# Optimization experiments

Hardware: AMD Instinct MI355X
Metric: run time of the kernel (lower is better)

## Reference

```python
import jax, jax.numpy as jnp
import numpy as np
from jax import lax


def _conv1d(x, w, b):
    # x: [B,C,W], w: [Cout,Cin,K], b: [Cout]; SAME padding for K=3
    k = w.shape[-1]
    pad = (k - 1) // 2
    y = lax.conv_general_dilated(
        x, w, window_strides=(1,), padding=[(pad, pad)],
        dimension_numbers=("NCH", "OIH", "NCH"))
    return y + b[None, :, None]


def setup_inputs() -> dict:
    key = jax.random.key(0)
    k1, k2 = jax.random.split(key)
    B, C, H, W = 8, 64, 256, 256
    K = 3
    X = jax.random.normal(k1, (B, C, H, W), dtype=jnp.float32)
    W_conv = jax.random.normal(k2, (C, C, K), dtype=jnp.float32) * (1.0 / np.sqrt(C * K))
    b_conv = jnp.zeros((C,), dtype=jnp.float32)
    return {"X": X, "W_conv": W_conv, "b_conv": b_conv}


def reference(X, W_conv, b_conv):
    # SpatialConv, direction='down', inplace=True:
    #   Y[0] = X[0];  Y[i+1] = X[i+1] + tanh(conv1d(Y[i]))
    # (inplace updates mean each step reads the already-updated previous row)
    rows = jnp.transpose(X, (2, 0, 1, 3))  # [H,B,C,W]

    def step(prev_row, x_next):
        new_row = x_next + jnp.tanh(_conv1d(prev_row, W_conv, b_conv))
        return new_row, new_row

    y0 = rows[0]
    _, ys = lax.scan(step, y0, rows[1:])  # ys: [H-1,B,C,W]
    Y = jnp.concatenate([y0[None], ys], axis=0)  # [H,B,C,W]
    return jnp.transpose(Y, (1, 2, 0, 3))  # [B,C,H,W]
```

## Files before the change

kernel.cpp:

```cpp
#include <hip/hip_runtime.h>

typedef __bf16 bf16x8 __attribute__((ext_vector_type(8)));
typedef __bf16 bf16x4 __attribute__((ext_vector_type(4)));
typedef float  f32x4  __attribute__((ext_vector_type(4)));

#define NB 8
#define NC 64
#define NH 256
#define NW 256
#define NT 16
#define WT 16
#define SEG 32
#define NS 5
#define LDSW 82
#define LDSC 72

__device__ __forceinline__ float fast_tanh(float x) {
    float e = __expf(2.0f * x);
    return 1.0f - 2.0f / (1.0f + e);
}

__global__ __launch_bounds__(256, 1)
void spconv_trap(const float* __restrict__ Xg,
                 const float* __restrict__ Wg,
                 const float* __restrict__ Bg,
                 float* __restrict__ Yg,
                 int* __restrict__ flags)
{
    const int b    = blockIdx.x & 7;
    const int t    = blockIdx.x >> 3;
    const int tid  = threadIdx.x;
    const int wv   = tid >> 6;
    const int lane = tid & 63;
    const int g    = lane >> 4;
    const int lm   = lane & 15;
    const int w0   = t * WT;
    const int wc0  = w0 - SEG;

    __shared__ __bf16 buf[2][LDSW][LDSC];

    bf16x8 afrag[6];
    {
        const int co = wv * 16 + lm;
        #pragma unroll
        for (int c = 0; c < 6; ++c) {
            const int k = c >> 1, ci0 = 32 * (c & 1) + 8 * g;
            bf16x8 a;
            #pragma unroll
            for (int j = 0; j < 8; ++j)
                a[j] = (__bf16)Wg[(co * NC + ci0 + j) * 3 + k];
            afrag[c] = a;
        }
    }
    float bias_r[4];
    #pragma unroll
    for (int i = 0; i < 4; ++i)
        bias_r[i] = Bg[wv * 16 + 4 * g + i];

    {
        const int ci = tid & 63;
        for (int r = (tid >> 6); r < LDSW; r += 4) {
            const int w = wc0 - 1 + r;
            float v = (w >= 0 && w < NW)
                    ? Xg[((size_t)(b * NC + ci) * NH + 0) * NW + w] : 0.0f;
            const __bf16 bv = (__bf16)v;
            buf[0][r][ci] = bv;
            buf[1][r][ci] = bv;
        }
    }
    #pragma unroll
    for (int i = 0; i < 4; ++i) {
        const int co = wv * 16 + 4 * g + i;
        const size_t idx = ((size_t)(b * NC + co) * NH + 0) * NW + w0 + lm;
        Yg[idx] = Xg[idx];
    }

    bool wok[NS];
    #pragma unroll
    for (int s = 0; s < NS; ++s) {
        const int w = wc0 + 16 * s + lm;
        wok[s] = (w >= 0 && w < NW);
    }

    float xA[NS][4], xB[NS][4];
    #pragma unroll
    for (int s = 0; s < NS; ++s)
        #pragma unroll
        for (int i = 0; i < 4; ++i) {
            const int co = wv * 16 + 4 * g + i;
            const int w  = wc0 + 16 * s + lm;
            xA[s][i] = wok[s]
                ? Xg[((size_t)(b * NC + co) * NH + 1) * NW + w] : 0.0f;
        }
    __syncthreads();

    const int myflag = b * NT + t;

    auto body = [&](int h, int p, float (&xcur)[NS][4], float (&xnext)[NS][4]) {
        if (h + 1 < NH) {
            #pragma unroll
            for (int s = 0; s < NS; ++s)
                #pragma unroll
                for (int i = 0; i < 4; ++i) {
                    const int co = wv * 16 + 4 * g + i;
                    const int w  = wc0 + 16 * s + lm;
                    xnext[s][i] = wok[s]
                        ? Xg[((size_t)(b * NC + co) * NH + h + 1) * NW + w] : 0.0f;
                }
        }

        float yv[NS][4];
        #pragma unroll
        for (int s = 0; s < NS; ++s) {
            f32x4 acc = {0.f, 0.f, 0.f, 0.f};
            #pragma unroll
            for (int c = 0; c < 6; ++c) {
                const bf16x8 bfr =
                    *(const bf16x8*)&buf[p][16 * s + lm + (c >> 1)][32 * (c & 1) + 8 * g];
                acc = __builtin_amdgcn_mfma_f32_16x16x32_bf16(afrag[c], bfr, acc, 0, 0, 0);
            }
            #pragma unroll
            for (int i = 0; i < 4; ++i)
                yv[s][i] = xcur[s][i] + fast_tanh(acc[i] + bias_r[i]);
        }
        #pragma unroll
        for (int i = 0; i < 4; ++i) {
            const int co = wv * 16 + 4 * g + i;
            Yg[((size_t)(b * NC + co) * NH + h) * NW + w0 + lm] = yv[SEG / 16][i];
        }

        #pragma unroll
        for (int s = 0; s < NS; ++s) {
            bf16x4 pk;
            #pragma unroll
            for (int i = 0; i < 4; ++i)
                pk[i] = wok[s] ? (__bf16)yv[s][i] : (__bf16)0.0f;
            *(bf16x4*)&buf[p ^ 1][16 * s + lm + 1][wv * 16 + 4 * g] = pk;
        }

        const bool boundary = (h < NH - 1) && ((h & (SEG - 1)) == 0);
        if (boundary) {
            const int k = h >> 5;
            __threadfence();
            __syncthreads();
            if (tid == 0)
                __hip_atomic_store(&flags[myflag], k,
                                   __ATOMIC_RELEASE, __HIP_MEMORY_SCOPE_AGENT);
            if (t > 0 && tid == 32) {
                while (__hip_atomic_load(&flags[myflag - 1], __ATOMIC_ACQUIRE,
                                         __HIP_MEMORY_SCOPE_AGENT) < k)
                    __builtin_amdgcn_s_sleep(2);
            }
            if (t < NT - 1 && tid == 96) {
                while (__hip_atomic_load(&flags[myflag + 1], __ATOMIC_ACQUIRE,
                                         __HIP_MEMORY_SCOPE_AGENT) < k)
                    __builtin_amdgcn_s_sleep(2);
            }
            __syncthreads();
            for (int idx = tid; idx < 2 * SEG * NC; idx += 256) {
                const int wloc = idx & 31;
                const int ci   = (idx >> 5) & 63;
                const int side = idx >> 11;
                const bool have = side ? (t < NT - 1) : (t > 0);
                if (have) {
                    const int w = w0 - SEG + wloc + side * (WT + SEG);
                    const int r = wloc + 1 + side * (WT + SEG);
                    buf[p ^ 1][r][ci] =
                        (__bf16)Yg[((size_t)(b * NC + ci) * NH + h) * NW + w];
                }
            }
            __syncthreads();
        } else {
            asm volatile("s_waitcnt lgkmcnt(0)" ::: "memory");
            __builtin_amdgcn_sched_barrier(0);
            __builtin_amdgcn_s_barrier();
            __builtin_amdgcn_sched_barrier(0);
        }
    };

    for (int h = 1; h < NH; h += 2) {
        body(h, 0, xA, xB);
        if (h + 1 < NH) body(h + 1, 1, xB, xA);
    }
}

extern "C" void kernel_launch(void* const* d_in, const int* in_sizes, int n_in,
                              void* d_out, int out_size, void* d_ws, size_t ws_size,
                              hipStream_t stream)
{
    const float* X  = (const float*)d_in[0];
    const float* Wc = (const float*)d_in[1];
    const float* Bc = (const float*)d_in[2];
    float* Y        = (float*)d_out;
    int* flags      = (int*)d_ws;

    hipMemsetAsync(d_ws, 0, NB * NT * sizeof(int), stream);

    dim3 grid(NB * NT);
    dim3 block(256);
    hipLaunchKernelGGL(spconv_trap, grid, block, 0, stream, X, Wc, Bc, Y, flags);
}
```

Baseline: 728.0 us.

## Split width sub-tiles across 8 waves and vectorize halo reload

Doubles the block to 512 threads so each output-channel group is handled by two waves, one taking the even and one the odd 16-wide sub-tiles. This cuts the per-wave serial MFMA, tanh and global-load work on each row of the sequential recurrence. The halo refill from global memory now uses 4-wide float loads instead of scalar loads. The cost is more waves meeting at each per-row barrier and an uneven split (3 sub-tiles versus 2), and the launch bounds change may alter register allocation.

```diff
diff --git a/kernel.cpp b/kernel.cpp
--- a/kernel.cpp
+++ b/kernel.cpp
@@ -20,7 +20,7 @@
     return 1.0f - 2.0f / (1.0f + e);
 }
 
-__global__ __launch_bounds__(256, 1)
+__global__ __launch_bounds__(512, 2)
 void spconv_trap(const float* __restrict__ Xg,
                  const float* __restrict__ Wg,
                  const float* __restrict__ Bg,
@@ -31,6 +31,10 @@
     const int t    = blockIdx.x >> 3;
     const int tid  = threadIdx.x;
     const int wv   = tid >> 6;
+    const int cot  = wv & 3;
+    const bool odd = wv >= 4;
+    const int sb   = odd ? 1 : 0;
+    const int nsub = odd ? 2 : 3;
     const int lane = tid & 63;
     const int g    = lane >> 4;
     const int lm   = lane & 15;
@@ -41,7 +45,7 @@
 
     bf16x8 afrag[6];
     {
-        const int co = wv * 16 + lm;
+        const int co = cot * 16 + lm;
         #pragma unroll
         for (int c = 0; c < 6; ++c) {
             const int k = c >> 1, ci0 = 32 * (c & 1) + 8 * g;
@@ -55,11 +59,11 @@
     float bias_r[4];
     #pragma unroll
     for (int i = 0; i < 4; ++i)
-        bias_r[i] = Bg[wv * 16 + 4 * g + i];
+        bias_r[i] = Bg[cot * 16 + 4 * g + i];
 
     {
         const int ci = tid & 63;
-        for (int r = (tid >> 6); r < LDSW; r += 4) {
+        for (int r = (tid >> 6); r < LDSW; r += 8) {
             const int w = wc0 - 1 + r;
             float v = (w >= 0 && w < NW)
                     ? Xg[((size_t)(b * NC + ci) * NH + 0) * NW + w] : 0.0f;
@@ -68,50 +72,58 @@
             buf[1][r][ci] = bv;
         }
     }
+    if (!odd) {
+        #pragma unroll
+        for (int i = 0; i < 4; ++i) {
+            const int co = cot * 16 + 4 * g + i;
+            const size_t idx = ((size_t)(b * NC + co) * NH + 0) * NW + w0 + lm;
+            Yg[idx] = Xg[idx];
+        }
+    }
+
+    bool wok[3];
     #pragma unroll
-    for (int i = 0; i < 4; ++i) {
-        const int co = wv * 16 + 4 * g + i;
-        const size_t idx = ((size_t)(b * NC + co) * NH + 0) * NW + w0 + lm;
-        Yg[idx] = Xg[idx];
-    }
-
-    bool wok[NS];
+    for (int j = 0; j < 3; ++j) {
+        const int s = 2 * j + sb;
+        const int w = wc0 + 16 * s + lm;
+        wok[j] = (w >= 0 && w < NW);
+    }
+
+    float xA[3][4], xB[3][4];
     #pragma unroll
-    for (int s = 0; s < NS; ++s) {
-        const int w = wc0 + 16 * s + lm;
-        wok[s] = (w >= 0 && w < NW);
-    }
-
-    float xA[NS][4], xB[NS][4];
-    #pragma unroll
-    for (int s = 0; s < NS; ++s)
+    for (int j = 0; j < 3; ++j) if (j < nsub) {
+        const int s = 2 * j + sb;
         #pragma unroll
         for (int i = 0; i < 4; ++i) {
-            const int co = wv * 16 + 4 * g + i;
+            const int co = cot * 16 + 4 * g + i;
             const int w  = wc0 + 16 * s + lm;
-            xA[s][i] = wok[s]
+            xA[j][i] = wok[j]
                 ? Xg[((size_t)(b * NC + co) * NH + 1) * NW + w] : 0.0f;
         }
+    }
     __syncthreads();
 
     const int myflag = b * NT + t;
 
-    auto body = [&](int h, int p, float (&xcur)[NS][4], float (&xnext)[NS][4]) {
+    auto body = [&](int h, int p, float (&xcur)[3][4], float (&xnext)[3][4]) {
         if (h + 1 < NH) {
             #pragma unroll
-            for (int s = 0; s < NS; ++s)
+            for (int j = 0; j < 3; ++j) if (j < nsub) {
+                const int s = 2 * j + sb;
                 #pragma unroll
                 for (int i = 0; i < 4; ++i) {
-                    const int co = wv * 16 + 4 * g + i;
+                    const int co = cot * 16 + 4 * g + i;
                     const int w  = wc0 + 16 * s + lm;
-                    xnext[s][i] = wok[s]
+                    xnext[j][i] = wok[j]
                         ? Xg[((size_t)(b * NC + co) * NH + h + 1) * NW + w] : 0.0f;
                 }
-        }
-
-        float yv[NS][4];
-        #pragma unroll
-        for (int s = 0; s < NS; ++s) {
+            }
+        }
+
+        float yv[3][4];
+        #pragma unroll
+        for (int j = 0; j < 3; ++j) if (j < nsub) {
+            const int s = 2 * j + sb;
             f32x4 acc = {0.f, 0.f, 0.f, 0.f};
             #pragma unroll
             for (int c = 0; c < 6; ++c) {
@@ -121,21 +133,24 @@
             }
             #pragma unroll
             for (int i = 0; i < 4; ++i)
-                yv[s][i] = xcur[s][i] + fast_tanh(acc[i] + bias_r[i]);
-        }
-        #pragma unroll
-        for (int i = 0; i < 4; ++i) {
-            const int co = wv * 16 + 4 * g + i;
-            Yg[((size_t)(b * NC + co) * NH + h) * NW + w0 + lm] = yv[SEG / 16][i];
-        }
-
-        #pragma unroll
-        for (int s = 0; s < NS; ++s) {
+                yv[j][i] = xcur[j][i] + fast_tanh(acc[i] + bias_r[i]);
+        }
+        if (!odd) {
+            #pragma unroll
+            for (int i = 0; i < 4; ++i) {
+                const int co = cot * 16 + 4 * g + i;
+                Yg[((size_t)(b * NC + co) * NH + h) * NW + w0 + lm] = yv[1][i];
+            }
+        }
+
+        #pragma unroll
+        for (int j = 0; j < 3; ++j) if (j < nsub) {
+            const int s = 2 * j + sb;
             bf16x4 pk;
             #pragma unroll
             for (int i = 0; i < 4; ++i)
-                pk[i] = wok[s] ? (__bf16)yv[s][i] : (__bf16)0.0f;
-            *(bf16x4*)&buf[p ^ 1][16 * s + lm + 1][wv * 16 + 4 * g] = pk;
+                pk[i] = wok[j] ? (__bf16)yv[j][i] : (__bf16)0.0f;
+            *(bf16x4*)&buf[p ^ 1][16 * s + lm + 1][cot * 16 + 4 * g] = pk;
         }
 
         const bool boundary = (h < NH - 1) && ((h & (SEG - 1)) == 0);
@@ -146,27 +161,30 @@
             if (tid == 0)
                 __hip_atomic_store(&flags[myflag], k,
                                    __ATOMIC_RELEASE, __HIP_MEMORY_SCOPE_AGENT);
-            if (t > 0 && tid == 32) {
+            if (t > 0 && tid == 64) {
                 while (__hip_atomic_load(&flags[myflag - 1], __ATOMIC_ACQUIRE,
                                          __HIP_MEMORY_SCOPE_AGENT) < k)
                     __builtin_amdgcn_s_sleep(2);
             }
-            if (t < NT - 1 && tid == 96) {
+            if (t < NT - 1 && tid == 448) {
                 while (__hip_atomic_load(&flags[myflag + 1], __ATOMIC_ACQUIRE,
                                          __HIP_MEMORY_SCOPE_AGENT) < k)
                     __builtin_amdgcn_s_sleep(2);
             }
             __syncthreads();
-            for (int idx = tid; idx < 2 * SEG * NC; idx += 256) {
-                const int wloc = idx & 31;
-                const int ci   = (idx >> 5) & 63;
-                const int side = idx >> 11;
+            for (int idx = tid; idx < 2 * NC * (SEG / 4); idx += 512) {
+                const int q    = idx & 7;
+                const int ci   = (idx >> 3) & 63;
+                const int side = idx >> 9;
                 const bool have = side ? (t < NT - 1) : (t > 0);
                 if (have) {
-                    const int w = w0 - SEG + wloc + side * (WT + SEG);
-                    const int r = wloc + 1 + side * (WT + SEG);
-                    buf[p ^ 1][r][ci] =
-                        (__bf16)Yg[((size_t)(b * NC + ci) * NH + h) * NW + w];
+                    const int wq = w0 - SEG + 4 * q + side * (WT + SEG);
+                    const int r  = 4 * q + 1 + side * (WT + SEG);
+                    const f32x4 v = *(const f32x4*)
+                        &Yg[((size_t)(b * NC + ci) * NH + h) * NW + wq];
+                    #pragma unroll
+                    for (int i2 = 0; i2 < 4; ++i2)
+                        buf[p ^ 1][r + i2][ci] = (__bf16)v[i2];
                 }
             }
             __syncthreads();
@@ -197,6 +215,6 @@
     hipMemsetAsync(d_ws, 0, NB * NT * sizeof(int), stream);
 
     dim3 grid(NB * NT);
-    dim3 block(256);
+    dim3 block(512);
     hipLaunchKernelGGL(spconv_trap, grid, block, 0, stream, X, Wc, Bc, Y, flags);
 }
```

Measured after the change: 879.0 us. 1.21x slower.

## Pack two column tiles per 512-thread block with LDS-atomic sub-barriers

Applied to the files above, without the earlier changes.

Each workgroup now holds two independent 256-thread tiles, so the grid shrinks from 128 to 64 blocks. The per-row s_barrier is replaced by a spin barrier on an LDS atomic counter, scoped to each half-block. The halo refill now reads four floats at a time. The aim is to fit two tiles per CU and cut per-block sync cost. In exchange, the LDS spin-waits may burn issue slots, and the counter is initialised without a barrier before first use, which risks a race.

```diff
diff --git a/kernel.cpp b/kernel.cpp
--- a/kernel.cpp
+++ b/kernel.cpp
@@ -20,7 +20,7 @@
     return 1.0f - 2.0f / (1.0f + e);
 }
 
-__global__ __launch_bounds__(256, 1)
+__global__ __launch_bounds__(512, 1)
 void spconv_trap(const float* __restrict__ Xg,
                  const float* __restrict__ Wg,
                  const float* __restrict__ Bg,
@@ -28,16 +28,22 @@
                  int* __restrict__ flags)
 {
     const int b    = blockIdx.x & 7;
-    const int t    = blockIdx.x >> 3;
+    const int q    = blockIdx.x >> 3;
     const int tid  = threadIdx.x;
-    const int wv   = tid >> 6;
+    const int jl   = tid >> 8;
+    const int jt   = tid & 255;
+    const int wv   = jt >> 6;
     const int lane = tid & 63;
     const int g    = lane >> 4;
     const int lm   = lane & 15;
+    const int t    = 2 * q + jl;
     const int w0   = t * WT;
     const int wc0  = w0 - SEG;
 
-    __shared__ __bf16 buf[2][LDSW][LDSC];
+    __shared__ __bf16 buf[2][2][LDSW][LDSC];
+    __shared__ int jctr[2][32];
+
+    if (tid < 2) jctr[tid][0] = 0;
 
     bf16x8 afrag[6];
     {
@@ -58,14 +64,14 @@
         bias_r[i] = Bg[wv * 16 + 4 * g + i];
 
     {
-        const int ci = tid & 63;
-        for (int r = (tid >> 6); r < LDSW; r += 4) {
+        const int ci = jt & 63;
+        for (int r = (jt >> 6); r < LDSW; r += 4) {
             const int w = wc0 - 1 + r;
             float v = (w >= 0 && w < NW)
                     ? Xg[((size_t)(b * NC + ci) * NH + 0) * NW + w] : 0.0f;
             const __bf16 bv = (__bf16)v;
-            buf[0][r][ci] = bv;
-            buf[1][r][ci] = bv;
+            buf[jl][0][r][ci] = bv;
+            buf[jl][1][r][ci] = bv;
         }
     }
     #pragma unroll
@@ -95,6 +101,20 @@
     __syncthreads();
 
     const int myflag = b * NT + t;
+
+    int ph = 0;
+    auto jbar = [&]() {
+        ++ph;
+        asm volatile("s_waitcnt lgkmcnt(0)" ::: "memory");
+        __builtin_amdgcn_sched_barrier(0);
+        if (lane == 0)
+            __hip_atomic_fetch_add(&jctr[jl][0], 1,
+                                   __ATOMIC_RELAXED, __HIP_MEMORY_SCOPE_WORKGROUP);
+        while (__hip_atomic_load(&jctr[jl][0],
+                                 __ATOMIC_RELAXED, __HIP_MEMORY_SCOPE_WORKGROUP)
+               < 4 * ph) {}
+        __builtin_amdgcn_sched_barrier(0);
+    };
 
     auto body = [&](int h, int p, float (&xcur)[NS][4], float (&xnext)[NS][4]) {
         if (h + 1 < NH) {
@@ -115,8 +135,8 @@
             f32x4 acc = {0.f, 0.f, 0.f, 0.f};
             #pragma unroll
             for (int c = 0; c < 6; ++c) {
-                const bf16x8 bfr =
-                    *(const bf16x8*)&buf[p][16 * s + lm + (c >> 1)][32 * (c & 1) + 8 * g];
+                const bf16x8 bfr = *(const bf16x8*)
+                    &buf[jl][p][16 * s + lm + (c >> 1)][32 * (c & 1) + 8 * g];
                 acc = __builtin_amdgcn_mfma_f32_16x16x32_bf16(afrag[c], bfr, acc, 0, 0, 0);
             }
             #pragma unroll
@@ -135,46 +155,46 @@
             #pragma unroll
             for (int i = 0; i < 4; ++i)
                 pk[i] = wok[s] ? (__bf16)yv[s][i] : (__bf16)0.0f;
-            *(bf16x4*)&buf[p ^ 1][16 * s + lm + 1][wv * 16 + 4 * g] = pk;
+            *(bf16x4*)&buf[jl][p ^ 1][16 * s + lm + 1][wv * 16 + 4 * g] = pk;
         }
 
         const bool boundary = (h < NH - 1) && ((h & (SEG - 1)) == 0);
         if (boundary) {
             const int k = h >> 5;
             __threadfence();
-            __syncthreads();
-            if (tid == 0)
+            jbar();
+            if (jt == 0)
                 __hip_atomic_store(&flags[myflag], k,
                                    __ATOMIC_RELEASE, __HIP_MEMORY_SCOPE_AGENT);
-            if (t > 0 && tid == 32) {
+            if (t > 0 && jt == 64) {
                 while (__hip_atomic_load(&flags[myflag - 1], __ATOMIC_ACQUIRE,
                                          __HIP_MEMORY_SCOPE_AGENT) < k)
                     __builtin_amdgcn_s_sleep(2);
             }
-            if (t < NT - 1 && tid == 96) {
+            if (t < NT - 1 && jt == 192) {
                 while (__hip_atomic_load(&flags[myflag + 1], __ATOMIC_ACQUIRE,
                                          __HIP_MEMORY_SCOPE_AGENT) < k)
                     __builtin_amdgcn_s_sleep(2);
             }
-            __syncthreads();
-            for (int idx = tid; idx < 2 * SEG * NC; idx += 256) {
-                const int wloc = idx & 31;
-                const int ci   = (idx >> 5) & 63;
-                const int side = idx >> 11;
+            jbar();
+            for (int idx = jt; idx < 2 * NC * (SEG / 4); idx += 256) {
+                const int q8   = idx & 7;
+                const int ci   = (idx >> 3) & 63;
+                const int side = idx >> 9;
                 const bool have = side ? (t < NT - 1) : (t > 0);
                 if (have) {
-                    const int w = w0 - SEG + wloc + side * (WT + SEG);
-                    const int r = wloc + 1 + side * (WT + SEG);
-                    buf[p ^ 1][r][ci] =
-                        (__bf16)Yg[((size_t)(b * NC + ci) * NH + h) * NW + w];
+                    const int wq = w0 - SEG + 4 * q8 + side * (WT + SEG);
+                    const int r  = 4 * q8 + 1 + side * (WT + SEG);
+                    const f32x4 v = *(const f32x4*)
+                        &Yg[((size_t)(b * NC + ci) * NH + h) * NW + wq];
+                    #pragma unroll
+                    for (int i2 = 0; i2 < 4; ++i2)
+                        buf[jl][p ^ 1][r + i2][ci] = (__bf16)v[i2];
                 }
             }
-            __syncthreads();
+            jbar();
         } else {
-            asm volatile("s_waitcnt lgkmcnt(0)" ::: "memory");
-            __builtin_amdgcn_sched_barrier(0);
-            __builtin_amdgcn_s_barrier();
-            __builtin_amdgcn_sched_barrier(0);
+            jbar();
         }
     };
 
@@ -196,7 +216,7 @@
 
     hipMemsetAsync(d_ws, 0, NB * NT * sizeof(int), stream);
 
-    dim3 grid(NB * NT);
-    dim3 block(256);
+    dim3 grid(NB * NT / 2);
+    dim3 block(512);
     hipLaunchKernelGGL(spconv_trap, grid, block, 0, stream, X, Wc, Bc, Y, flags);
 }
```

After: 980.7 us. 1.35x slower.

## Repartition MFMA work so each wave owns a width strip across all output channels

Applied to the files above, without the earlier changes.

Each wave used to compute 16 output channels across all five width segments. Now it computes all 64 output channels for its own 16-wide width strip, plus a 16-channel slice of the shared fifth segment. This reduces the LDS B-fragment reads per wave, since one set of fragments is reused across four channel tiles. In exchange each wave holds all four weight fragment sets in registers (24 bf16x8 instead of 6), which raises register pressure, and only wave 2 writes the output row.

```diff
diff --git a/kernel.cpp b/kernel.cpp
--- a/kernel.cpp
+++ b/kernel.cpp
@@ -39,9 +39,10 @@
 
     __shared__ __bf16 buf[2][LDSW][LDSC];
 
-    bf16x8 afrag[6];
-    {
-        const int co = wv * 16 + lm;
+    bf16x8 afrag[4][6];
+    #pragma unroll
+    for (int ct = 0; ct < 4; ++ct) {
+        const int co = ct * 16 + lm;
         #pragma unroll
         for (int c = 0; c < 6; ++c) {
             const int k = c >> 1, ci0 = 32 * (c & 1) + 8 * g;
@@ -49,13 +50,15 @@
             #pragma unroll
             for (int j = 0; j < 8; ++j)
                 a[j] = (__bf16)Wg[(co * NC + ci0 + j) * 3 + k];
-            afrag[c] = a;
-        }
-    }
-    float bias_r[4];
-    #pragma unroll
-    for (int i = 0; i < 4; ++i)
-        bias_r[i] = Bg[wv * 16 + 4 * g + i];
+            afrag[ct][c] = a;
+        }
+    }
+    float bias_r[4][4];
+    #pragma unroll
+    for (int ct = 0; ct < 4; ++ct)
+        #pragma unroll
+        for (int i = 0; i < 4; ++i)
+            bias_r[ct][i] = Bg[ct * 16 + 4 * g + i];
 
     {
         const int ci = tid & 63;
@@ -75,67 +78,105 @@
         Yg[idx] = Xg[idx];
     }
 
-    bool wok[NS];
-    #pragma unroll
-    for (int s = 0; s < NS; ++s) {
-        const int w = wc0 + 16 * s + lm;
-        wok[s] = (w >= 0 && w < NW);
-    }
-
-    float xA[NS][4], xB[NS][4];
-    #pragma unroll
-    for (int s = 0; s < NS; ++s)
+    const int wp = wc0 + 16 * wv + lm;
+    const int ws = wc0 + 64 + lm;
+    const bool wokp = (wp >= 0 && wp < NW);
+    const bool woks = (ws >= 0 && ws < NW);
+
+    float xA[5][4], xB[5][4];
+    #pragma unroll
+    for (int ct = 0; ct < 4; ++ct)
         #pragma unroll
         for (int i = 0; i < 4; ++i) {
-            const int co = wv * 16 + 4 * g + i;
-            const int w  = wc0 + 16 * s + lm;
-            xA[s][i] = wok[s]
-                ? Xg[((size_t)(b * NC + co) * NH + 1) * NW + w] : 0.0f;
-        }
+            const int co = ct * 16 + 4 * g + i;
+            xA[ct][i] = wokp
+                ? Xg[((size_t)(b * NC + co) * NH + 1) * NW + wp] : 0.0f;
+        }
+    #pragma unroll
+    for (int i = 0; i < 4; ++i) {
+        const int co = wv * 16 + 4 * g + i;
+        xA[4][i] = woks
+            ? Xg[((size_t)(b * NC + co) * NH + 1) * NW + ws] : 0.0f;
+    }
     __syncthreads();
 
     const int myflag = b * NT + t;
 
-    auto body = [&](int h, int p, float (&xcur)[NS][4], float (&xnext)[NS][4]) {
+    auto body = [&](int h, int p, float (&xcur)[5][4], float (&xnext)[5][4]) {
         if (h + 1 < NH) {
             #pragma unroll
-            for (int s = 0; s < NS; ++s)
+            for (int ct = 0; ct < 4; ++ct)
                 #pragma unroll
                 for (int i = 0; i < 4; ++i) {
-                    const int co = wv * 16 + 4 * g + i;
-                    const int w  = wc0 + 16 * s + lm;
-                    xnext[s][i] = wok[s]
-                        ? Xg[((size_t)(b * NC + co) * NH + h + 1) * NW + w] : 0.0f;
+                    const int co = ct * 16 + 4 * g + i;
+                    xnext[ct][i] = wokp
+                        ? Xg[((size_t)(b * NC + co) * NH + h + 1) * NW + wp] : 0.0f;
                 }
-        }
-
-        float yv[NS][4];
-        #pragma unroll
-        for (int s = 0; s < NS; ++s) {
+            #pragma unroll
+            for (int i = 0; i < 4; ++i) {
+                const int co = wv * 16 + 4 * g + i;
+                xnext[4][i] = woks
+                    ? Xg[((size_t)(b * NC + co) * NH + h + 1) * NW + ws] : 0.0f;
+            }
+        }
+
+        bf16x8 bfrp[6], bfrs[6];
+        #pragma unroll
+        for (int c = 0; c < 6; ++c)
+            bfrp[c] = *(const bf16x8*)
+                &buf[p][16 * wv + lm + (c >> 1)][32 * (c & 1) + 8 * g];
+        #pragma unroll
+        for (int c = 0; c < 6; ++c)
+            bfrs[c] = *(const bf16x8*)
+                &buf[p][64 + lm + (c >> 1)][32 * (c & 1) + 8 * g];
+
+        float yp[4][4], ys[4];
+        #pragma unroll
+        for (int ct = 0; ct < 4; ++ct) {
             f32x4 acc = {0.f, 0.f, 0.f, 0.f};
             #pragma unroll
-            for (int c = 0; c < 6; ++c) {
-                const bf16x8 bfr =
-                    *(const bf16x8*)&buf[p][16 * s + lm + (c >> 1)][32 * (c & 1) + 8 * g];
-                acc = __builtin_amdgcn_mfma_f32_16x16x32_bf16(afrag[c], bfr, acc, 0, 0, 0);
-            }
-            #pragma unroll
-            for (int i = 0; i < 4; ++i)
-                yv[s][i] = xcur[s][i] + fast_tanh(acc[i] + bias_r[i]);
-        }
-        #pragma unroll
-        for (int i = 0; i < 4; ++i) {
-            const int co = wv * 16 + 4 * g + i;
-            Yg[((size_t)(b * NC + co) * NH + h) * NW + w0 + lm] = yv[SEG / 16][i];
-        }
-
-        #pragma unroll
-        for (int s = 0; s < NS; ++s) {
+            for (int c = 0; c < 6; ++c)
+                acc = __builtin_amdgcn_mfma_f32_16x16x32_bf16(
+                        afrag[ct][c], bfrp[c], acc, 0, 0, 0);
+            #pragma unroll
+            for (int i = 0; i < 4; ++i)
+                yp[ct][i] = xcur[ct][i] + fast_tanh(acc[i] + bias_r[ct][i]);
+        }
+        {
+            f32x4 acc = {0.f, 0.f, 0.f, 0.f};
+            #pragma unroll
+            for (int c = 0; c < 6; ++c)
+                acc = __builtin_amdgcn_mfma_f32_16x16x32_bf16(
+                        afrag[wv][c], bfrs[c], acc, 0, 0, 0);
+            #pragma unroll
+            for (int i = 0; i < 4; ++i)
+                ys[i] = xcur[4][i] + fast_tanh(acc[i] + bias_r[wv][i]);
+        }
+
+        if (wv == 2) {
+            #pragma unroll
+            for (int ct = 0; ct < 4; ++ct)
+                #pragma unroll
+                for (int i = 0; i < 4; ++i) {
+                    const int co = ct * 16 + 4 * g + i;
+                    Yg[((size_t)(b * NC + co) * NH + h) * NW + w0 + lm] = yp[ct][i];
+                }
+        }
+
+        #pragma unroll
+        for (int ct = 0; ct < 4; ++ct) {
             bf16x4 pk;
             #pragma unroll
             for (int i = 0; i < 4; ++i)
-                pk[i] = wok[s] ? (__bf16)yv[s][i] : (__bf16)0.0f;
-            *(bf16x4*)&buf[p ^ 1][16 * s + lm + 1][wv * 16 + 4 * g] = pk;
+                pk[i] = wokp ? (__bf16)yp[ct][i] : (__bf16)0.0f;
+            *(bf16x4*)&buf[p ^ 1][16 * wv + lm + 1][ct * 16 + 4 * g] = pk;
+        }
+        {
+            bf16x4 pk;
+            #pragma unroll
+            for (int i = 0; i < 4; ++i)
+                pk[i] = woks ? (__bf16)ys[i] : (__bf16)0.0f;
+            *(bf16x4*)&buf[p ^ 1][64 + lm + 1][wv * 16 + 4 * g] = pk;
         }
 
         const bool boundary = (h < NH - 1) && ((h & (SEG - 1)) == 0);
```

Result: slower. 993.4 us (+36.4%).
